# Kernel optimization log

Hardware: AMD Instinct MI355X
Metric: run time of the kernel (lower is better)

The kernel has to match this reference:

```python
import jax, jax.numpy as jnp
import numpy as np

BS, VARNUM, EMB_DIM, SEED_DIM, N_HEADS = 32, 16384, 128, 128, 16


def setup_inputs() -> dict:
    key = jax.random.key(0)
    k1, k2, k3, k4 = jax.random.split(key, 4)
    query_seed = jax.random.normal(k1, (BS, SEED_DIM), dtype=jnp.float32)
    embeddings = jax.random.normal(k2, (BS, VARNUM, EMB_DIM), dtype=jnp.float32)
    # mask over varnum//2 base variables; 1 = keep, 0 = mask out
    attn_mask = jax.random.randint(k3, (BS, VARNUM // 2), 0, 2, dtype=jnp.int32)
    # xavier_normal_ init: std = sqrt(2 / (fan_in + fan_out))
    xavier_std = float(np.sqrt(2.0 / (EMB_DIM + SEED_DIM)))
    w_qs = jax.random.normal(k4, (N_HEADS, EMB_DIM, SEED_DIM), dtype=jnp.float32) * xavier_std
    return {"query_seed": query_seed, "embeddings": embeddings,
            "attn_mask": attn_mask, "w_qs": w_qs}


def _l2_normalize(x):
    # x / ||x||_2 along last dim (no eps, matching torch source)
    return x / jnp.linalg.norm(x, axis=-1, keepdims=True)


def reference(query_seed, embeddings, attn_mask, w_qs):
    bs, varnum, emb_dim = embeddings.shape
    n_heads = w_qs.shape[0]

    norm_embs = _l2_normalize(embeddings)                      # [bs, varnum, emb]
    # mm(w_qs.view(-1, seed), seed.T).T.view(bs, n_heads, emb) == einsum
    qs = jnp.tanh(jnp.einsum("hes,bs->bhe", w_qs, query_seed))  # [bs, heads, emb]
    norm_qs = _l2_normalize(qs)

    # orthogonality loss between head queries
    gram = jnp.einsum("bhe,bge->bhg", norm_qs, norm_qs)        # [bs, h, h]
    diff = gram - jnp.eye(n_heads, dtype=gram.dtype)
    loss = jnp.sum(diff * diff) / bs

    # cosine-similarity attention
    attn = jnp.einsum("bhe,bve->bhv", norm_qs, norm_embs)      # [bs, h, varnum]
    mask_full = jnp.concatenate([attn_mask, attn_mask], axis=1)[:, None, :]  # [bs,1,varnum]
    attn = jnp.where(mask_full == 0, -jnp.inf, attn)
    final_attn = jax.nn.softmax(attn, axis=-1)
    rc = jnp.einsum("bhv,bve->bhe", final_attn, embeddings)    # values = embeddings
    return rc, loss
```

## Files before the change

kernel.cpp:

```cpp
#include <hip/hip_runtime.h>
#include <hip/hip_bf16.h>
#include <cstdint>

#define BS     32
#define VARNUM 16384
#define EMB    128
#define SEEDD  128
#define NH     16
#define HALFV  8192

#define NCHUNK 32
#define VT     (VARNUM / NCHUNK)
#define TV     64
#define NTILE  (VT / TV)

#define EST 2080
#define PST 144

#define OFF_NORMQ 0
#define SZ_NORMQ  (BS*NH*EMB*4)
#define OFF_LOSSP (OFF_NORMQ + SZ_NORMQ)
#define SZ_LOSSP  256
#define OFF_LPART (OFF_LOSSP + SZ_LOSSP)
#define SZ_LPART  (BS*NCHUNK*NH*4)
#define OFF_PACC  (OFF_LPART + SZ_LPART)
#define SZ_PACC   ((size_t)BS*NCHUNK*NH*EMB*4)

typedef __attribute__((ext_vector_type(8))) short bf16x8;
typedef __attribute__((ext_vector_type(4))) float f32x4;

static __device__ __forceinline__ uint16_t f2bf(float f) {
    uint32_t u = __float_as_uint(f);
    return (uint16_t)((u + 0x7FFFu + ((u >> 16) & 1u)) >> 16);
}
static __device__ __forceinline__ uint32_t packbf(float a, float b) {
    __hip_bfloat162 h = __float22bfloat162_rn(make_float2(a, b));
    uint32_t u;
    __builtin_memcpy(&u, &h, 4);
    return u;
}
static __device__ __forceinline__ float dot4(float4 a, float4 b) {
    return a.x*b.x + a.y*b.y + a.z*b.z + a.w*b.w;
}

__global__ __launch_bounds__(128) void k1_q(const float* __restrict__ seed,
                                            const float* __restrict__ wqs,
                                            float* __restrict__ normq) {
    const int bh = blockIdx.x;
    const int b = bh >> 4, h = bh & 15;
    const int e = threadIdx.x;
    __shared__ __align__(16) float s_seed[SEEDD];
    s_seed[e] = seed[b*SEEDD + e];
    __syncthreads();
    const float4* w4 = (const float4*)(wqs + ((size_t)(h*EMB + e))*SEEDD);
    const float4* s4 = (const float4*)s_seed;
    float acc = 0.f;
    #pragma unroll
    for (int j = 0; j < SEEDD/4; ++j) acc += dot4(w4[j], s4[j]);
    float t = tanhf(acc);
    float sq = t*t;
    #pragma unroll
    for (int off = 32; off; off >>= 1) sq += __shfl_xor(sq, off);
    __shared__ float s_part[2];
    if ((threadIdx.x & 63) == 0) s_part[threadIdx.x >> 6] = sq;
    __syncthreads();
    float tot = s_part[0] + s_part[1];
    normq[((size_t)b*NH + h)*EMB + e] = t * rsqrtf(tot);
}

__global__ __launch_bounds__(256) void k2_loss(const float* __restrict__ normq,
                                               float* __restrict__ lossp) {
    const int b = blockIdx.x;
    const int h = threadIdx.x >> 4, g = threadIdx.x & 15;
    const float4* qh = (const float4*)(normq + ((size_t)b*NH + h)*EMB);
    const float4* qg = (const float4*)(normq + ((size_t)b*NH + g)*EMB);
    float d = 0.f;
    #pragma unroll
    for (int j = 0; j < EMB/4; ++j) d += dot4(qh[j], qg[j]);
    d -= (h == g) ? 1.f : 0.f;
    float sq = d*d;
    #pragma unroll
    for (int off = 32; off; off >>= 1) sq += __shfl_xor(sq, off);
    __shared__ float sp[4];
    if ((threadIdx.x & 63) == 0) sp[threadIdx.x >> 6] = sq;
    __syncthreads();
    if (threadIdx.x == 0) lossp[b] = sp[0] + sp[1] + sp[2] + sp[3];
}

__global__ __launch_bounds__(256) void k_fused(const float* __restrict__ emb,
                                               const int* __restrict__ mask,
                                               const float* __restrict__ normq,
                                               float* __restrict__ pacc,
                                               float* __restrict__ lpart) {
    const int chunk = blockIdx.x, b = blockIdx.y;
    const int tid = threadIdx.x;
    const int w   = tid >> 6;
    const int l   = tid & 63;
    const int lhi = l >> 4;
    const int llo = l & 15;

    __shared__ __align__(16) unsigned char Elds[8*EST];
    __shared__ __align__(16) unsigned char Plds[16*PST];
    __shared__ __align__(16) float nsq[TV];
    __shared__ float lred[4][NH];

    bf16x8 qf[4];
    {
        const float* qrow = normq + ((size_t)b*NH + llo)*EMB;
        #pragma unroll
        for (int f = 0; f < 4; ++f) {
            const float4* qs = (const float4*)(qrow + f*32 + lhi*8);
            float4 a = qs[0], c = qs[1];
            bf16x8 t;
            t[0]=(short)f2bf(a.x); t[1]=(short)f2bf(a.y); t[2]=(short)f2bf(a.z); t[3]=(short)f2bf(a.w);
            t[4]=(short)f2bf(c.x); t[5]=(short)f2bf(c.y); t[6]=(short)f2bf(c.z); t[7]=(short)f2bf(c.w);
            qf[f] = t;
        }
    }

    f32x4 acc0 = {0.f,0.f,0.f,0.f};
    f32x4 acc1 = {0.f,0.f,0.f,0.f};
    float Lh = 0.f;

    const float* embB  = emb + (size_t)b*VARNUM*EMB;
    const int*   maskB = mask + b*HALFV;
    const int    r0    = tid >> 4;
    const int    cb    = tid & 15;

    for (int t = 0; t < NTILE; ++t) {
        const int vg0 = chunk*VT + t*TV;

        #pragma unroll
        for (int rep = 0; rep < 4; ++rep) {
            const int row = rep*16 + r0;
            const int vg  = vg0 + row;
            const int mk  = maskB[vg & (HALFV-1)];
            const float4* src = (const float4*)(embB + (size_t)(mk ? vg : vg0)*EMB + cb*8);
            float4 x0 = src[0], x1 = src[1];
            float sq = dot4(x0,x0) + dot4(x1,x1);
            sq += __shfl_xor(sq, 1); sq += __shfl_xor(sq, 2);
            sq += __shfl_xor(sq, 4); sq += __shfl_xor(sq, 8);
            if (cb == 0) nsq[row] = mk ? sq : 0.f;
            uint32_t d0 = packbf(x0.x, x0.y), d1 = packbf(x0.z, x0.w);
            uint32_t d2 = packbf(x1.x, x1.y), d3 = packbf(x1.z, x1.w);
            *(uint4*)(Elds + (cb>>1)*EST + row*32 + (cb&1)*16) = make_uint4(d0,d1,d2,d3);
        }
        __syncthreads();

        f32x4 s = {0.f,0.f,0.f,0.f};
        #pragma unroll
        for (int f = 0; f < 4; ++f) {
            const int eblk = 2*f + (lhi >> 1);
            bf16x8 a = *(const bf16x8*)(Elds + eblk*EST + (w*16 + llo)*32 + (lhi&1)*16);
            s = __builtin_amdgcn_mfma_f32_16x16x32_bf16(a, qf[f], s, 0, 0, 0);
        }
        f32x4 nn = *(const f32x4*)(&nsq[w*16 + lhi*4]);
        float p[4];
        #pragma unroll
        for (int r = 0; r < 4; ++r)
            p[r] = (nn[r] > 0.f) ? __expf(s[r]*rsqrtf(nn[r]) - 1.f) : 0.f;
        uint32_t u0 = packbf(p[0], p[1]), u1 = packbf(p[2], p[3]);
        Lh += __uint_as_float(u0 << 16) + __uint_as_float(u0 & 0xFFFF0000u)
            + __uint_as_float(u1 << 16) + __uint_as_float(u1 & 0xFFFF0000u);
        {
            unsigned char* pdst = Plds + llo*PST + (w*16 + lhi*4)*2;
            *(uint32_t*)(pdst)     = u0;
            *(uint32_t*)(pdst + 4) = u1;
        }
        __syncthreads();

        #pragma unroll
        for (int kf = 0; kf < 2; ++kf) {
            bf16x8 pa = *(const bf16x8*)(Plds + llo*PST + kf*64 + lhi*16);
            #pragma unroll
            for (int et = 0; et < 2; ++et) {
                const unsigned char* base = Elds + (w*2 + et)*EST + llo*2;
                bf16x8 bb;
                #pragma unroll
                for (int i = 0; i < 8; ++i)
                    bb[i] = *(const short*)(base + (size_t)(kf*32 + lhi*8 + i)*32);
                if (et == 0) acc0 = __builtin_amdgcn_mfma_f32_16x16x32_bf16(pa, bb, acc0, 0, 0, 0);
                else         acc1 = __builtin_amdgcn_mfma_f32_16x16x32_bf16(pa, bb, acc1, 0, 0, 0);
            }
        }
        __syncthreads();
    }

    float* pout = pacc + (((size_t)b*NCHUNK + chunk)*NH)*EMB;
    #pragma unroll
    for (int r = 0; r < 4; ++r) {
        pout[(lhi*4 + r)*EMB + w*32 + llo]      = acc0[r];
        pout[(lhi*4 + r)*EMB + w*32 + 16 + llo] = acc1[r];
    }
    Lh += __shfl_xor(Lh, 16);
    Lh += __shfl_xor(Lh, 32);
    if (l < 16) lred[w][l] = Lh;
    __syncthreads();
    if (tid < 16)
        lpart[((size_t)b*NCHUNK + chunk)*NH + tid] =
            lred[0][tid] + lred[1][tid] + lred[2][tid] + lred[3][tid];
}

__global__ __launch_bounds__(128) void k6_out(const float* __restrict__ pacc,
                                              const float* __restrict__ lpart,
                                              float* __restrict__ out) {
    const int bh = blockIdx.x;
    const int b = bh >> 4, h = bh & 15;
    const int e = threadIdx.x;
    float L = 0.f;
    #pragma unroll
    for (int c = 0; c < NCHUNK; ++c) L += lpart[((size_t)b*NCHUNK + c)*NH + h];
    float acc = 0.f;
    for (int k = 0; k < NCHUNK; ++k)
        acc += pacc[(((size_t)b*NCHUNK + k)*NH + h)*EMB + e];
    out[((size_t)b*NH + h)*EMB + e] = acc / L;
}

__global__ __launch_bounds__(64) void k_loss(const float* __restrict__ lossp,
                                             float* __restrict__ out) {
    const int l = threadIdx.x;
    float v = (l < BS) ? lossp[l] : 0.f;
    #pragma unroll
    for (int off = 32; off; off >>= 1) v += __shfl_xor(v, off);
    if (l == 0) out[BS*NH*EMB] = v / (float)BS;
}

extern "C" void kernel_launch(void* const* d_in, const int* in_sizes, int n_in,
                              void* d_out, int out_size, void* d_ws, size_t ws_size,
                              hipStream_t stream) {
    const float* seed = (const float*)d_in[0];
    const float* emb  = (const float*)d_in[1];
    const int*   mask = (const int*)d_in[2];
    const float* wqs  = (const float*)d_in[3];
    float* out = (float*)d_out;

    char* ws = (char*)d_ws;
    float* normq = (float*)(ws + OFF_NORMQ);
    float* lossp = (float*)(ws + OFF_LOSSP);
    float* lpart = (float*)(ws + OFF_LPART);
    float* pacc  = (float*)(ws + OFF_PACC);

    k1_q<<<BS*NH, 128, 0, stream>>>(seed, wqs, normq);
    k2_loss<<<BS, 256, 0, stream>>>(normq, lossp);
    k_fused<<<dim3(NCHUNK, BS), 256, 0, stream>>>(emb, mask, normq, pacc, lpart);
    k6_out<<<BS*NH, 128, 0, stream>>>(pacc, lpart, out);
    k_loss<<<1, 64, 0, stream>>>(lossp, out);
}
```

Baseline: 62.85 us.

## Register-prefetch next embedding tile during MFMA compute in fused attention kernel

Loads the next tile's mask values and embedding rows into registers before computing the current tile, so global memory latency overlaps the MFMA scoring and softmax-accumulate work. It also adds a min-blocks-per-CU hint of 4 to launch_bounds. The prefetch buffers add about 32 VGPRs per thread, which together with the occupancy hint may cause spills or lower occupancy.

```diff
diff --git a/kernel.cpp b/kernel.cpp
--- a/kernel.cpp
+++ b/kernel.cpp
@@ -87,11 +87,11 @@
     if (threadIdx.x == 0) lossp[b] = sp[0] + sp[1] + sp[2] + sp[3];
 }
 
-__global__ __launch_bounds__(256) void k_fused(const float* __restrict__ emb,
-                                               const int* __restrict__ mask,
-                                               const float* __restrict__ normq,
-                                               float* __restrict__ pacc,
-                                               float* __restrict__ lpart) {
+__global__ __launch_bounds__(256, 4) void k_fused(const float* __restrict__ emb,
+                                                  const int* __restrict__ mask,
+                                                  const float* __restrict__ normq,
+                                                  float* __restrict__ pacc,
+                                                  float* __restrict__ lpart) {
     const int chunk = blockIdx.x, b = blockIdx.y;
     const int tid = threadIdx.x;
     const int w   = tid >> 6;
@@ -127,25 +127,55 @@
     const int    r0    = tid >> 4;
     const int    cb    = tid & 15;
 
+    int    mk[4];
+    float4 pfa[4], pfb[4];
+    {
+        const int vg00 = chunk*VT;
+        #pragma unroll
+        for (int rep = 0; rep < 4; ++rep)
+            mk[rep] = maskB[(vg00 + rep*16 + r0) & (HALFV-1)];
+        #pragma unroll
+        for (int rep = 0; rep < 4; ++rep) {
+            const int vg = vg00 + rep*16 + r0;
+            const float4* src = (const float4*)(embB + (size_t)(mk[rep] ? vg : vg00)*EMB + cb*8);
+            pfa[rep] = src[0]; pfb[rep] = src[1];
+        }
+    }
+
     for (int t = 0; t < NTILE; ++t) {
-        const int vg0 = chunk*VT + t*TV;
+        const int vg0  = chunk*VT + t*TV;
+        const int vg0n = vg0 + TV;
+
+        int mkn[4];
+        if (t + 1 < NTILE) {
+            #pragma unroll
+            for (int rep = 0; rep < 4; ++rep)
+                mkn[rep] = maskB[(vg0n + rep*16 + r0) & (HALFV-1)];
+        }
 
         #pragma unroll
         for (int rep = 0; rep < 4; ++rep) {
             const int row = rep*16 + r0;
-            const int vg  = vg0 + row;
-            const int mk  = maskB[vg & (HALFV-1)];
-            const float4* src = (const float4*)(embB + (size_t)(mk ? vg : vg0)*EMB + cb*8);
-            float4 x0 = src[0], x1 = src[1];
+            float4 x0 = pfa[rep], x1 = pfb[rep];
             float sq = dot4(x0,x0) + dot4(x1,x1);
             sq += __shfl_xor(sq, 1); sq += __shfl_xor(sq, 2);
             sq += __shfl_xor(sq, 4); sq += __shfl_xor(sq, 8);
-            if (cb == 0) nsq[row] = mk ? sq : 0.f;
+            if (cb == 0) nsq[row] = mk[rep] ? sq : 0.f;
             uint32_t d0 = packbf(x0.x, x0.y), d1 = packbf(x0.z, x0.w);
             uint32_t d2 = packbf(x1.x, x1.y), d3 = packbf(x1.z, x1.w);
             *(uint4*)(Elds + (cb>>1)*EST + row*32 + (cb&1)*16) = make_uint4(d0,d1,d2,d3);
         }
         __syncthreads();
+
+        if (t + 1 < NTILE) {
+            #pragma unroll
+            for (int rep = 0; rep < 4; ++rep) {
+                const int vg = vg0n + rep*16 + r0;
+                const float4* src = (const float4*)(embB + (size_t)(mkn[rep] ? vg : vg0n)*EMB + cb*8);
+                pfa[rep] = src[0]; pfb[rep] = src[1];
+                mk[rep]  = mkn[rep];
+            }
+        }
 
         f32x4 s = {0.f,0.f,0.f,0.f};
         #pragma unroll
```

Result: faster. 53.53 us (-14.8%).
